# Kernel tuning notes

Measured on AMD Instinct MI355X. Metric: run time of the kernel, lower is better.

Reference implementation:

```python
import jax, jax.numpy as jnp
import numpy as np

N = 40000          # nodes
E = 640000         # edges (avg degree 16)
D = 128            # in_channels == out_channels
G = 8              # graphs
NPG = N // G       # nodes per graph
EPS = 1e-6
SLOPE = 0.01       # torch LeakyReLU default


def leaky(x):
    return jnp.where(x >= 0, x, SLOPE * x)


def setup_inputs() -> dict:
    key = jax.random.key(0)
    ks = jax.random.split(key, 8)
    x = jax.random.normal(ks[0], (N, D), dtype=jnp.float32)
    edge_index = jax.random.randint(ks[1], (2, E), 0, N, dtype=jnp.int32)
    w = jax.random.uniform(ks[2], (E, 1), dtype=jnp.float32)
    batch = jnp.repeat(jnp.arange(G, dtype=jnp.int32), NPG)
    batch_num = jnp.full((G,), NPG, dtype=jnp.int32)
    s = 1.0 / np.sqrt(D)
    W1 = jax.random.uniform(ks[3], (D, D), jnp.float32, -s, s)
    W2 = jax.random.uniform(ks[4], (D, D), jnp.float32, -s, s)
    Wo = jax.random.uniform(ks[5], (D, D), jnp.float32, -s, s)
    Wn = jax.random.uniform(ks[6], (D, D), jnp.float32, -s, s)
    gamma = jnp.ones((D,), jnp.float32)
    beta = jnp.zeros((D,), jnp.float32)
    return {"x": x, "edge_index": edge_index, "w": w, "batch": batch,
            "batch_num": batch_num, "W1": W1, "W2": W2, "Wo": Wo, "Wn": Wn,
            "gamma": gamma, "beta": beta}


def reference(x, edge_index, w, batch, batch_num, W1, W2, Wo, Wn, gamma, beta):
    # mlp_x (dropout in eval mode => identity)
    h = leaky(x @ W1) @ W2                                    # [N, D]
    # gather -> scale -> scatter-sum -> activate
    xj = w * h[edge_index[1]]                                 # [E, D]
    xn = leaky(jax.ops.segment_sum(xj, edge_index[0], num_segments=N))
    out = h @ Wo + xn @ Wn                                    # [N, D]
    # GraphNorm: per-graph mean and unbiased std (torch_scatter defaults)
    cnt = batch_num.astype(jnp.float32)[:, None]              # [G, 1]
    mu = jax.ops.segment_sum(out, batch, num_segments=G) / cnt
    diff = out - mu[batch]
    var = jax.ops.segment_sum(diff * diff, batch, num_segments=G) / (cnt - 1.0)
    sigma = jnp.sqrt(var)
    return diff / (sigma[batch] + EPS) * gamma + beta
```

## Files before the change

kernel.cpp:

```cpp
#include <hip/hip_runtime.h>
#include <hip/hip_bf16.h>

#define D 128
#define NN 40000
#define EE 640000
#define GG 8
#define NPG 5000
#define CSUB 16
#define OVCAP 4095
#define REP 32

using short8 = __attribute__((ext_vector_type(8))) short;
using f32x4 = __attribute__((ext_vector_type(4))) float;

__device__ __forceinline__ float lrelu(float v) { return v >= 0.f ? v : 0.01f * v; }

__device__ __forceinline__ ushort f2bf(float f) {
    union { float f; uint u; } c; c.f = f;
    return (ushort)((c.u + 0x7FFFu + ((c.u >> 16) & 1u)) >> 16);
}
__device__ __forceinline__ float bf2f_lo(uint u) { union { uint u; float f; } c; c.u = u << 16; return c.f; }
__device__ __forceinline__ float bf2f_hi(uint u) { union { uint u; float f; } c; c.u = u & 0xFFFF0000u; return c.f; }

__global__ __launch_bounds__(256) void prep_k(const float* __restrict__ W1,
                                              const float* __restrict__ W2,
                                              const float* __restrict__ Wo,
                                              const float* __restrict__ Wn,
                                              short* __restrict__ WT,
                                              uint4* __restrict__ zbase, int zlen16) {
    const int b = blockIdx.x;
    if (b < 4) {
        const float* W = b == 0 ? W1 : b == 1 ? W2 : b == 2 ? Wo : Wn;
        short* T = WT + b * (D * D);
#pragma unroll 4
        for (int i = 0; i < 64; ++i) {
            int flat = threadIdx.x + i * 256;
            int k = flat >> 7, n = flat & 127;
            T[n * D + k] = (short)f2bf(W[flat]);
        }
    } else {
        int idx = (b - 4) * 256 + threadIdx.x;
        if (idx < zlen16) zbase[idx] = uint4{0, 0, 0, 0};
    }
}

__device__ __forceinline__ void stage_B(const short* __restrict__ WT,
                                        short (*Bs)[136], int tid) {
    const uint4* bsrc = (const uint4*)WT;
#pragma unroll
    for (int i = 0; i < 8; ++i) {
        int idx = tid + i * 256;
        int flat = idx * 8;
        *(uint4*)&Bs[flat >> 7][flat & 127] = bsrc[idx];
    }
}

__device__ __forceinline__ void mfma8(const short8 (&a)[4], short (*Bs)[136],
                                      f32x4 (&acc)[8], int lrow, int kgrp) {
#pragma unroll
    for (int ks = 0; ks < 4; ++ks) {
        const int kb = ks * 32 + kgrp;
#pragma unroll
        for (int nt = 0; nt < 8; ++nt) {
            short8 b = *(const short8*)&Bs[nt * 16 + lrow][kb];
            acc[nt] = __builtin_amdgcn_mfma_f32_16x16x32_bf16(a[ks], b, acc[nt], 0, 0, 0);
        }
    }
}

__global__ __launch_bounds__(256) void mlpfill_k(const float* __restrict__ x,
                                                 const short* __restrict__ W1T,
                                                 const short* __restrict__ W2T,
                                                 ushort* __restrict__ h,
                                                 const int* __restrict__ ei,
                                                 const float* __restrict__ w,
                                                 int* __restrict__ deg4,
                                                 int2* __restrict__ csr,
                                                 int* __restrict__ ov) {
    __shared__ short Bs[128][136];
    __shared__ short tw[4][16][136];
    const int tid = threadIdx.x;
    if (blockIdx.x < NN / 64) {
        const int wv = tid >> 6, lane = tid & 63;
        const int lrow = lane & 15, kgrp = (lane >> 4) * 8;
        const int m0 = wv * 16;
        const int arow = blockIdx.x * 64;
        short8 a[4];
#pragma unroll
        for (int ks = 0; ks < 4; ++ks) {
            const float* xp = &x[(size_t)(arow + m0 + lrow) * D + ks * 32 + kgrp];
            const float4 u0 = *(const float4*)xp;
            const float4 u1 = *(const float4*)(xp + 4);
            short8 aa;
            aa[0] = (short)f2bf(u0.x); aa[1] = (short)f2bf(u0.y);
            aa[2] = (short)f2bf(u0.z); aa[3] = (short)f2bf(u0.w);
            aa[4] = (short)f2bf(u1.x); aa[5] = (short)f2bf(u1.y);
            aa[6] = (short)f2bf(u1.z); aa[7] = (short)f2bf(u1.w);
            a[ks] = aa;
        }
        stage_B(W1T, Bs, tid);
        __syncthreads();
        f32x4 acc[8] = {};
        mfma8(a, Bs, acc, lrow, kgrp);
        const int c0 = lane & 15;
        const int rg = (lane >> 4) * 4;
#pragma unroll
        for (int nt = 0; nt < 8; ++nt)
#pragma unroll
            for (int r = 0; r < 4; ++r)
                tw[wv][rg + r][nt * 16 + c0] = (short)f2bf(lrelu(acc[nt][r]));
        __syncthreads();
        stage_B(W2T, Bs, tid);
#pragma unroll
        for (int ks = 0; ks < 4; ++ks)
            a[ks] = *(const short8*)&tw[wv][lrow][ks * 32 + kgrp];
#pragma unroll
        for (int nt = 0; nt < 8; ++nt) acc[nt] = f32x4{0.f, 0.f, 0.f, 0.f};
        __syncthreads();
        mfma8(a, Bs, acc, lrow, kgrp);
#pragma unroll
        for (int nt = 0; nt < 8; ++nt)
#pragma unroll
            for (int r = 0; r < 4; ++r)
                h[(size_t)(arow + m0 + rg + r) * D + nt * 16 + c0] = f2bf(acc[nt][r]);
    } else {
        const int t = (blockIdx.x - NN / 64) * 256 + tid;
        const int e0 = t * 4;
        const int4 dst = *(const int4*)&ei[e0];
        const int4 src = *(const int4*)&ei[EE + e0];
        const float4 wv4 = *(const float4*)&w[e0];
        const int ds[4] = {dst.x, dst.y, dst.z, dst.w};
        const int sr[4] = {src.x, src.y, src.z, src.w};
        const float wf[4] = {wv4.x, wv4.y, wv4.z, wv4.w};
        int pos[4];
#pragma unroll
        for (int k = 0; k < 4; ++k) pos[k] = atomicAdd(&deg4[k * NN + ds[k]], 1);
#pragma unroll
        for (int k = 0; k < 4; ++k) {
            if (pos[k] < CSUB) {
                csr[(size_t)ds[k] * 64 + k * CSUB + pos[k]] = make_int2(sr[k], __float_as_int(wf[k]));
            } else {
                const int oi = atomicAdd(&ov[0], 1);
                if (oi < OVCAP) ov[1 + oi] = e0 + k;
            }
        }
    }
}

__global__ __launch_bounds__(256) void gather_k(const ushort* __restrict__ h,
                                                const int* __restrict__ deg4,
                                                const int2* __restrict__ csr,
                                                const int* __restrict__ ei,
                                                const float* __restrict__ w,
                                                const int* __restrict__ ov,
                                                ushort* __restrict__ xnact) {
    const int n = blockIdx.x * 16 + (threadIdx.x >> 4);
    const int lane = threadIdx.x & 15;
    const int d0 = deg4[0 * NN + n], d1 = deg4[1 * NN + n];
    const int d2 = deg4[2 * NN + n], d3 = deg4[3 * NN + n];
    const int c0 = min(d0, CSUB), c1 = min(d1, CSUB);
    const int c2 = min(d2, CSUB), c3 = min(d3, CSUB);
    const int t0 = c0, t1 = t0 + c1, t2 = t1 + c2;
    const int total = t2 + c3;
    const int2* row = csr + (size_t)n * 64;
    float acc[8] = {};
    int j = 0;
    for (; j + 8 <= total; j += 8) {
        int2 p[8]; uint4 v[8];
#pragma unroll
        for (int t = 0; t < 8; ++t) {
            const int jj = j + t;
            const int s = jj < t0 ? jj
                        : jj < t1 ? jj - t0 + CSUB
                        : jj < t2 ? jj - t1 + 2 * CSUB
                                  : jj - t2 + 3 * CSUB;
            p[t] = row[s];
        }
#pragma unroll
        for (int t = 0; t < 8; ++t) v[t] = *((const uint4*)(h + (size_t)p[t].x * D) + lane);
#pragma unroll
        for (int t = 0; t < 8; ++t) {
            const float wv = __int_as_float(p[t].y);
            acc[0] += wv * bf2f_lo(v[t].x); acc[1] += wv * bf2f_hi(v[t].x);
            acc[2] += wv * bf2f_lo(v[t].y); acc[3] += wv * bf2f_hi(v[t].y);
            acc[4] += wv * bf2f_lo(v[t].z); acc[5] += wv * bf2f_hi(v[t].z);
            acc[6] += wv * bf2f_lo(v[t].w); acc[7] += wv * bf2f_hi(v[t].w);
        }
    }
    if (j + 4 <= total) {
        int2 p[4]; uint4 v[4];
#pragma unroll
        for (int t = 0; t < 4; ++t) {
            const int jj = j + t;
            const int s = jj < t0 ? jj
                        : jj < t1 ? jj - t0 + CSUB
                        : jj < t2 ? jj - t1 + 2 * CSUB
                                  : jj - t2 + 3 * CSUB;
            p[t] = row[s];
        }
#pragma unroll
        for (int t = 0; t < 4; ++t) v[t] = *((const uint4*)(h + (size_t)p[t].x * D) + lane);
#pragma unroll
        for (int t = 0; t < 4; ++t) {
            const float wv = __int_as_float(p[t].y);
            acc[0] += wv * bf2f_lo(v[t].x); acc[1] += wv * bf2f_hi(v[t].x);
            acc[2] += wv * bf2f_lo(v[t].y); acc[3] += wv * bf2f_hi(v[t].y);
            acc[4] += wv * bf2f_lo(v[t].z); acc[5] += wv * bf2f_hi(v[t].z);
            acc[6] += wv * bf2f_lo(v[t].w); acc[7] += wv * bf2f_hi(v[t].w);
        }
        j += 4;
    }
    for (; j < total; ++j) {
        const int s = j < t0 ? j
                    : j < t1 ? j - t0 + CSUB
                    : j < t2 ? j - t1 + 2 * CSUB
                             : j - t2 + 3 * CSUB;
        const int2 p = row[s];
        const uint4 v = *((const uint4*)(h + (size_t)p.x * D) + lane);
        const float wv = __int_as_float(p.y);
        acc[0] += wv * bf2f_lo(v.x); acc[1] += wv * bf2f_hi(v.x);
        acc[2] += wv * bf2f_lo(v.y); acc[3] += wv * bf2f_hi(v.y);
        acc[4] += wv * bf2f_lo(v.z); acc[5] += wv * bf2f_hi(v.z);
        acc[6] += wv * bf2f_lo(v.w); acc[7] += wv * bf2f_hi(v.w);
    }
    if (d0 > CSUB || d1 > CSUB || d2 > CSUB || d3 > CSUB) {
        const int cnt = min(ov[0], OVCAP);
        for (int i = 0; i < cnt; ++i) {
            const int e = ov[1 + i];
            if (ei[e] == n) {
                const float wv = w[e];
                const uint4 v = *((const uint4*)(h + (size_t)ei[EE + e] * D) + lane);
                acc[0] += wv * bf2f_lo(v.x); acc[1] += wv * bf2f_hi(v.x);
                acc[2] += wv * bf2f_lo(v.y); acc[3] += wv * bf2f_hi(v.y);
                acc[4] += wv * bf2f_lo(v.z); acc[5] += wv * bf2f_hi(v.z);
                acc[6] += wv * bf2f_lo(v.w); acc[7] += wv * bf2f_hi(v.w);
            }
        }
    }
    uint4 st;
    st.x = (uint)f2bf(lrelu(acc[0])) | ((uint)f2bf(lrelu(acc[1])) << 16);
    st.y = (uint)f2bf(lrelu(acc[2])) | ((uint)f2bf(lrelu(acc[3])) << 16);
    st.z = (uint)f2bf(lrelu(acc[4])) | ((uint)f2bf(lrelu(acc[5])) << 16);
    st.w = (uint)f2bf(lrelu(acc[6])) | ((uint)f2bf(lrelu(acc[7])) << 16);
    *((uint4*)(xnact + (size_t)n * D) + lane) = st;
}

__global__ __launch_bounds__(256) void mmstats_k(const ushort* __restrict__ h,
                                                 const short* __restrict__ WoT,
                                                 const ushort* __restrict__ xa,
                                                 const short* __restrict__ WnT,
                                                 float* __restrict__ out,
                                                 float* __restrict__ statsR) {
    __shared__ short Bs[128][136];
    __shared__ float ls[2][16][132];
    const int tid = threadIdx.x;
    const int wv = tid >> 6, lane = tid & 63;
    const int lrow = lane & 15, kgrp = (lane >> 4) * 8;
    const int m0 = wv * 16;
    const int arow = blockIdx.x * 64;
    short8 a[4];
#pragma unroll
    for (int ks = 0; ks < 4; ++ks)
        a[ks] = *(const short8*)&h[(size_t)(arow + m0 + lrow) * D + ks * 32 + kgrp];
    stage_B(WoT, Bs, tid);
    __syncthreads();
    f32x4 acc[8] = {};
    mfma8(a, Bs, acc, lrow, kgrp);
#pragma unroll
    for (int ks = 0; ks < 4; ++ks)
        a[ks] = *(const short8*)&xa[(size_t)(arow + m0 + lrow) * D + ks * 32 + kgrp];
    __syncthreads();
    stage_B(WnT, Bs, tid);
    __syncthreads();
    mfma8(a, Bs, acc, lrow, kgrp);
    const int c0 = lane & 15;
    const int rg = (lane >> 4) * 4;
    const int li = wv * 4 + (lane >> 4);
#pragma unroll
    for (int nt = 0; nt < 8; ++nt) {
        float s = 0.f, q = 0.f;
#pragma unroll
        for (int r = 0; r < 4; ++r) {
            const float v = acc[nt][r];
            out[(size_t)(arow + m0 + rg + r) * D + nt * 16 + c0] = v;
            s += v; q += v * v;
        }
        ls[0][li][nt * 16 + c0] = s;
        ls[1][li][nt * 16 + c0] = q;
    }
    __syncthreads();
    if (tid < 128) {
        const int g0 = arow / NPG;
        const int gsplit = (g0 + 1) * NPG - arow;
        float s0 = 0.f, q0 = 0.f, s1 = 0.f, q1 = 0.f;
#pragma unroll
        for (int i = 0; i < 16; ++i) {
            const float sv = ls[0][i][tid];
            const float qv = ls[1][i][tid];
            if (i * 4 >= gsplit) { s1 += sv; q1 += qv; }
            else { s0 += sv; q0 += qv; }
        }
        const int rep = blockIdx.x & (REP - 1);
        float* S = &statsR[(size_t)rep * (2 * GG * D) + 0 * GG * D + g0 * D + tid];
        float* Q = &statsR[(size_t)rep * (2 * GG * D) + 1 * GG * D + g0 * D + tid];
        atomicAdd(S, s0);
        atomicAdd(Q, q0);
        if (gsplit < 64) { atomicAdd(S + D, s1); atomicAdd(Q + D, q1); }
    }
}

__global__ __launch_bounds__(256) void reduce_k(const float* __restrict__ statsR,
                                                float* __restrict__ statsF) {
    const int idx = blockIdx.x * 256 + threadIdx.x;
    float s = 0.f;
#pragma unroll
    for (int rep = 0; rep < REP; ++rep) s += statsR[rep * (2 * GG * D) + idx];
    statsF[idx] = s;
}

__global__ __launch_bounds__(256) void norm_k(float* __restrict__ out,
                                              const float* __restrict__ statsF,
                                              const float* __restrict__ gamma,
                                              const float* __restrict__ beta) {
    const int i4 = blockIdx.x * 256 + threadIdx.x;
    const int row = i4 >> 5;
    const int g = row / NPG;
    const int d0 = (i4 & 31) * 4;
    float4 v = *((float4*)out + i4);
    const float4 s4 = *(const float4*)&statsF[g * D + d0];
    const float4 q4 = *(const float4*)&statsF[GG * D + g * D + d0];
    const float4 g4 = *(const float4*)&gamma[d0];
    const float4 b4 = *(const float4*)&beta[d0];
    const float inv = 1.f / (float)NPG;
    const float invm1 = 1.f / (float)(NPG - 1);
    float mu, var, sg;
    mu = s4.x * inv; var = (q4.x - s4.x * mu) * invm1; sg = sqrtf(fmaxf(var, 0.f));
    v.x = (v.x - mu) / (sg + 1e-6f) * g4.x + b4.x;
    mu = s4.y * inv; var = (q4.y - s4.y * mu) * invm1; sg = sqrtf(fmaxf(var, 0.f));
    v.y = (v.y - mu) / (sg + 1e-6f) * g4.y + b4.y;
    mu = s4.z * inv; var = (q4.z - s4.z * mu) * invm1; sg = sqrtf(fmaxf(var, 0.f));
    v.z = (v.z - mu) / (sg + 1e-6f) * g4.z + b4.z;
    mu = s4.w * inv; var = (q4.w - s4.w * mu) * invm1; sg = sqrtf(fmaxf(var, 0.f));
    v.w = (v.w - mu) / (sg + 1e-6f) * g4.w + b4.w;
    *((float4*)out + i4) = v;
}

extern "C" void kernel_launch(void* const* d_in, const int* in_sizes, int n_in,
                              void* d_out, int out_size, void* d_ws, size_t ws_size,
                              hipStream_t stream) {
    const float* x = (const float*)d_in[0];
    const int* ei = (const int*)d_in[1];
    const float* w = (const float*)d_in[2];
    const float* W1 = (const float*)d_in[5];
    const float* W2 = (const float*)d_in[6];
    const float* Wo = (const float*)d_in[7];
    const float* Wn = (const float*)d_in[8];
    const float* gamma = (const float*)d_in[9];
    const float* beta = (const float*)d_in[10];
    float* out = (float*)d_out;

    char* ws = (char*)d_ws;
    const size_t BF16MAT = (size_t)NN * D * 2;
    size_t off = 0;
    ushort* h = (ushort*)(ws + off);      off += BF16MAT;
    ushort* xnact = (ushort*)(ws + off);  off += BF16MAT;
    const size_t ZOFF = off;
    float* statsR = (float*)(ws + off);   off += (size_t)REP * 2 * GG * D * 4;
    float* statsF = (float*)(ws + off);   off += 2 * GG * D * 4;
    int* deg4 = (int*)(ws + off);         off += (size_t)NN * 4 * 4;
    int* ov = (int*)(ws + off);           off += (1 + OVCAP) * 4;
    const int ZLEN16 = (int)((off - ZOFF) / 16);
    short* WT = (short*)(ws + off);       off += 4 * (size_t)D * D * 2;
    int2* csr = (int2*)(ws + off);

    prep_k<<<4 + (ZLEN16 + 255) / 256, 256, 0, stream>>>(W1, W2, Wo, Wn, WT,
                                                         (uint4*)(ws + ZOFF), ZLEN16);
    mlpfill_k<<<2 * (NN / 64), 256, 0, stream>>>(x, WT, WT + D * D, h,
                                                 ei, w, deg4, csr, ov);
    gather_k<<<NN / 16, 256, 0, stream>>>(h, deg4, csr, ei, w, ov, xnact);
    mmstats_k<<<NN / 64, 256, 0, stream>>>(h, WT + 2 * D * D, xnact, WT + 3 * D * D, out, statsR);
    reduce_k<<<(2 * GG * D) / 256, 256, 0, stream>>>(statsR, statsF);
    norm_k<<<(NN * D / 4) / 256, 256, 0, stream>>>(out, statsF, gamma, beta);
}
```

Before: 193.9 us.

## Split MLP and CSR fill kernels; use 512-thread MLP blocks with global intermediate

Splits the combined MLP and edge-fill kernel into two separate launches. The MLP kernel now uses 512-thread blocks covering 128 rows and stages the leaky-ReLU intermediate through a global scratch buffer instead of shared memory. This halves how often each block loads the weight tiles into shared memory and removes the branch-divergent mixed kernel. In exchange it adds a kernel launch, extra global traffic for the intermediate, and loses the overlap of fill atomics with the MLP.

After: 197.1 us. About the same (+1.7%).

```diff
diff --git a/kernel.cpp b/kernel.cpp
--- a/kernel.cpp
+++ b/kernel.cpp
@@ -44,12 +44,13 @@
     }
 }
 
+template <int NT>
 __device__ __forceinline__ void stage_B(const short* __restrict__ WT,
                                         short (*Bs)[136], int tid) {
     const uint4* bsrc = (const uint4*)WT;
 #pragma unroll
-    for (int i = 0; i < 8; ++i) {
-        int idx = tid + i * 256;
+    for (int i = 0; i < 2048 / NT; ++i) {
+        int idx = tid + i * NT;
         int flat = idx * 8;
         *(uint4*)&Bs[flat >> 7][flat & 127] = bsrc[idx];
     }
@@ -68,81 +69,84 @@
     }
 }
 
-__global__ __launch_bounds__(256) void mlpfill_k(const float* __restrict__ x,
-                                                 const short* __restrict__ W1T,
-                                                 const short* __restrict__ W2T,
-                                                 ushort* __restrict__ h,
-                                                 const int* __restrict__ ei,
-                                                 const float* __restrict__ w,
-                                                 int* __restrict__ deg4,
-                                                 int2* __restrict__ csr,
-                                                 int* __restrict__ ov) {
+__global__ __launch_bounds__(512) void mlp_k(const float* __restrict__ x,
+                                             const short* __restrict__ W1T,
+                                             const short* __restrict__ W2T,
+                                             ushort* __restrict__ t1g,
+                                             ushort* __restrict__ h) {
     __shared__ short Bs[128][136];
-    __shared__ short tw[4][16][136];
     const int tid = threadIdx.x;
-    if (blockIdx.x < NN / 64) {
-        const int wv = tid >> 6, lane = tid & 63;
-        const int lrow = lane & 15, kgrp = (lane >> 4) * 8;
-        const int m0 = wv * 16;
-        const int arow = blockIdx.x * 64;
-        short8 a[4];
-#pragma unroll
-        for (int ks = 0; ks < 4; ++ks) {
-            const float* xp = &x[(size_t)(arow + m0 + lrow) * D + ks * 32 + kgrp];
-            const float4 u0 = *(const float4*)xp;
-            const float4 u1 = *(const float4*)(xp + 4);
-            short8 aa;
-            aa[0] = (short)f2bf(u0.x); aa[1] = (short)f2bf(u0.y);
-            aa[2] = (short)f2bf(u0.z); aa[3] = (short)f2bf(u0.w);
-            aa[4] = (short)f2bf(u1.x); aa[5] = (short)f2bf(u1.y);
-            aa[6] = (short)f2bf(u1.z); aa[7] = (short)f2bf(u1.w);
-            a[ks] = aa;
-        }
-        stage_B(W1T, Bs, tid);
-        __syncthreads();
-        f32x4 acc[8] = {};
-        mfma8(a, Bs, acc, lrow, kgrp);
-        const int c0 = lane & 15;
-        const int rg = (lane >> 4) * 4;
-#pragma unroll
-        for (int nt = 0; nt < 8; ++nt)
-#pragma unroll
-            for (int r = 0; r < 4; ++r)
-                tw[wv][rg + r][nt * 16 + c0] = (short)f2bf(lrelu(acc[nt][r]));
-        __syncthreads();
-        stage_B(W2T, Bs, tid);
-#pragma unroll
-        for (int ks = 0; ks < 4; ++ks)
-            a[ks] = *(const short8*)&tw[wv][lrow][ks * 32 + kgrp];
-#pragma unroll
-        for (int nt = 0; nt < 8; ++nt) acc[nt] = f32x4{0.f, 0.f, 0.f, 0.f};
-        __syncthreads();
-        mfma8(a, Bs, acc, lrow, kgrp);
-#pragma unroll
-        for (int nt = 0; nt < 8; ++nt)
-#pragma unroll
-            for (int r = 0; r < 4; ++r)
-                h[(size_t)(arow + m0 + rg + r) * D + nt * 16 + c0] = f2bf(acc[nt][r]);
-    } else {
-        const int t = (blockIdx.x - NN / 64) * 256 + tid;
-        const int e0 = t * 4;
-        const int4 dst = *(const int4*)&ei[e0];
-        const int4 src = *(const int4*)&ei[EE + e0];
-        const float4 wv4 = *(const float4*)&w[e0];
-        const int ds[4] = {dst.x, dst.y, dst.z, dst.w};
-        const int sr[4] = {src.x, src.y, src.z, src.w};
-        const float wf[4] = {wv4.x, wv4.y, wv4.z, wv4.w};
-        int pos[4];
-#pragma unroll
-        for (int k = 0; k < 4; ++k) pos[k] = atomicAdd(&deg4[k * NN + ds[k]], 1);
-#pragma unroll
-        for (int k = 0; k < 4; ++k) {
-            if (pos[k] < CSUB) {
-                csr[(size_t)ds[k] * 64 + k * CSUB + pos[k]] = make_int2(sr[k], __float_as_int(wf[k]));
-            } else {
-                const int oi = atomicAdd(&ov[0], 1);
-                if (oi < OVCAP) ov[1 + oi] = e0 + k;
-            }
+    const int wv = tid >> 6, lane = tid & 63;
+    const int lrow = lane & 15, kgrp = (lane >> 4) * 8;
+    const int arowm = blockIdx.x * 128 + wv * 16;
+    const int rA = min(arowm + lrow, NN - 1);
+    short8 a[4];
+#pragma unroll
+    for (int ks = 0; ks < 4; ++ks) {
+        const float* xp = &x[(size_t)rA * D + ks * 32 + kgrp];
+        const float4 u0 = *(const float4*)xp;
+        const float4 u1 = *(const float4*)(xp + 4);
+        short8 aa;
+        aa[0] = (short)f2bf(u0.x); aa[1] = (short)f2bf(u0.y);
+        aa[2] = (short)f2bf(u0.z); aa[3] = (short)f2bf(u0.w);
+        aa[4] = (short)f2bf(u1.x); aa[5] = (short)f2bf(u1.y);
+        aa[6] = (short)f2bf(u1.z); aa[7] = (short)f2bf(u1.w);
+        a[ks] = aa;
+    }
+    stage_B<512>(W1T, Bs, tid);
+    __syncthreads();
+    f32x4 acc[8] = {};
+    mfma8(a, Bs, acc, lrow, kgrp);
+    const int c0 = lane & 15;
+    const int rg = (lane >> 4) * 4;
+#pragma unroll
+    for (int nt = 0; nt < 8; ++nt)
+#pragma unroll
+        for (int r = 0; r < 4; ++r) {
+            const int row = arowm + rg + r;
+            if (row < NN) t1g[(size_t)row * D + nt * 16 + c0] = f2bf(lrelu(acc[nt][r]));
+        }
+    __syncthreads();
+    stage_B<512>(W2T, Bs, tid);
+#pragma unroll
+    for (int ks = 0; ks < 4; ++ks)
+        a[ks] = *(const short8*)&t1g[(size_t)rA * D + ks * 32 + kgrp];
+#pragma unroll
+    for (int nt = 0; nt < 8; ++nt) acc[nt] = f32x4{0.f, 0.f, 0.f, 0.f};
+    __syncthreads();
+    mfma8(a, Bs, acc, lrow, kgrp);
+#pragma unroll
+    for (int nt = 0; nt < 8; ++nt)
+#pragma unroll
+        for (int r = 0; r < 4; ++r) {
+            const int row = arowm + rg + r;
+            if (row < NN) h[(size_t)row * D + nt * 16 + c0] = f2bf(acc[nt][r]);
+        }
+}
+
+__global__ __launch_bounds__(256) void fill_k(const int* __restrict__ ei,
+                                              const float* __restrict__ w,
+                                              int* __restrict__ deg4,
+                                              int2* __restrict__ csr,
+                                              int* __restrict__ ov) {
+    const int t = blockIdx.x * 256 + threadIdx.x;
+    const int e0 = t * 4;
+    const int4 dst = *(const int4*)&ei[e0];
+    const int4 src = *(const int4*)&ei[EE + e0];
+    const float4 wv4 = *(const float4*)&w[e0];
+    const int ds[4] = {dst.x, dst.y, dst.z, dst.w};
+    const int sr[4] = {src.x, src.y, src.z, src.w};
+    const float wf[4] = {wv4.x, wv4.y, wv4.z, wv4.w};
+    int pos[4];
+#pragma unroll
+    for (int k = 0; k < 4; ++k) pos[k] = atomicAdd(&deg4[k * NN + ds[k]], 1);
+#pragma unroll
+    for (int k = 0; k < 4; ++k) {
+        if (pos[k] < CSUB) {
+            csr[(size_t)ds[k] * 64 + k * CSUB + pos[k]] = make_int2(sr[k], __float_as_int(wf[k]));
+        } else {
+            const int oi = atomicAdd(&ov[0], 1);
+            if (oi < OVCAP) ov[1 + oi] = e0 + k;
         }
     }
 }
@@ -262,7 +266,7 @@
 #pragma unroll
     for (int ks = 0; ks < 4; ++ks)
         a[ks] = *(const short8*)&h[(size_t)(arow + m0 + lrow) * D + ks * 32 + kgrp];
-    stage_B(WoT, Bs, tid);
+    stage_B<256>(WoT, Bs, tid);
     __syncthreads();
     f32x4 acc[8] = {};
     mfma8(a, Bs, acc, lrow, kgrp);
@@ -270,7 +274,7 @@
     for (int ks = 0; ks < 4; ++ks)
         a[ks] = *(const short8*)&xa[(size_t)(arow + m0 + lrow) * D + ks * 32 + kgrp];
     __syncthreads();
-    stage_B(WnT, Bs, tid);
+    stage_B<256>(WnT, Bs, tid);
     __syncthreads();
     mfma8(a, Bs, acc, lrow, kgrp);
     const int c0 = lane & 15;
@@ -371,12 +375,13 @@
     int* ov = (int*)(ws + off);           off += (1 + OVCAP) * 4;
     const int ZLEN16 = (int)((off - ZOFF) / 16);
     short* WT = (short*)(ws + off);       off += 4 * (size_t)D * D * 2;
-    int2* csr = (int2*)(ws + off);
+    int2* csr = (int2*)(ws + off);        off += (size_t)NN * 64 * 8;
+    ushort* t1g = (ushort*)(ws + off);
 
     prep_k<<<4 + (ZLEN16 + 255) / 256, 256, 0, stream>>>(W1, W2, Wo, Wn, WT,
                                                          (uint4*)(ws + ZOFF), ZLEN16);
-    mlpfill_k<<<2 * (NN / 64), 256, 0, stream>>>(x, WT, WT + D * D, h,
-                                                 ei, w, deg4, csr, ov);
+    fill_k<<<EE / (256 * 4), 256, 0, stream>>>(ei, w, deg4, csr, ov);
+    mlp_k<<<(NN + 127) / 128, 512, 0, stream>>>(x, WT, WT + D * D, t1g, h);
     gather_k<<<NN / 16, 256, 0, stream>>>(h, deg4, csr, ei, w, ov, xnact);
     mmstats_k<<<NN / 64, 256, 0, stream>>>(h, WT + 2 * D * D, xnact, WT + 3 * D * D, out, statsR);
     reduce_k<<<(2 * GG * D) / 256, 256, 0, stream>>>(statsR, statsF);
```
